# Performance work log

Measured on AMD Instinct MI355X. Metric: run time of the kernel, lower is better.

The kernel has to match this reference:

```python
import jax, jax.numpy as jnp
import numpy as np

N, E, B = 4096, 8192, 128


def seg_softmax(logits, seg, n):
    m = jax.ops.segment_max(logits, seg, num_segments=n)
    e = jnp.exp(logits - m[seg])
    s = jax.ops.segment_sum(e, seg, num_segments=n)
    return e / (s[seg] + 1e-16)


def gat(x, src, dst, W, a_src, a_dst, b, H, C, n):
    # PyG GATConv, concat=False (mean over heads), self-loops already appended
    h = (x @ W).reshape(n, H, C)
    al_s = jnp.sum(h * a_src, -1)  # [n,H]
    al_d = jnp.sum(h * a_dst, -1)
    logits = jax.nn.leaky_relu(al_s[src] + al_d[dst], 0.2)  # [E',H]
    alpha = seg_softmax(logits, dst, n)
    out = jax.ops.segment_sum(h[src] * alpha[:, :, None], dst, num_segments=n)
    return out.mean(1) + b


def gcn(x, src, dst, W, b, n):
    deg = jax.ops.segment_sum(jnp.ones_like(dst, jnp.float32), dst, num_segments=n)
    dis = jnp.where(deg > 0, deg ** -0.5, 0.0)
    norm = dis[src] * dis[dst]
    h = x @ W
    return jax.ops.segment_sum(h[src] * norm[:, None], dst, num_segments=n) + b


def transformer_conv(x, src, dst, Wq, bq, Wk, bk, Wv, bv, Ws, bs, H, C, n):
    # PyG TransformerConv, concat=False, root_weight=True, no self-loops
    q = (x @ Wq + bq).reshape(n, H, C)
    k = (x @ Wk + bk).reshape(n, H, C)
    v = (x @ Wv + bv).reshape(n, H, C)
    logits = jnp.sum(q[dst] * k[src], -1) / jnp.sqrt(jnp.float32(C))  # [E,H]
    alpha = seg_softmax(logits, dst, n)
    agg = jax.ops.segment_sum(v[src] * alpha[:, :, None], dst, num_segments=n)
    return agg.mean(1) + (x @ Ws + bs)


def gap(x, batch, nb):
    s = jax.ops.segment_sum(x, batch, num_segments=nb)
    cnt = jax.ops.segment_sum(jnp.ones(x.shape[0], x.dtype), batch, num_segments=nb)
    return s / jnp.maximum(cnt, 1.0)[:, None]


def setup_inputs() -> dict:
    key = jax.random.key(0)
    ks = iter(jax.random.split(key, 64))
    p = {}
    p['x'] = jax.random.normal(next(ks), (N, 78), jnp.float32)
    p['fp'] = (jax.random.uniform(next(ks), (B, 1489)) > 0.5).astype(jnp.float32)
    p['edge_index'] = jax.random.randint(next(ks), (2, E), 0, N, jnp.int32)
    p['batch'] = (jnp.arange(N, dtype=jnp.int32) // (N // B))
    def w(k, shp, fan):
        return jax.random.normal(k, shp, jnp.float32) * (1.0 / np.sqrt(fan))
    # GAT layers (in, out, heads=8)
    for name, ci, co in [('g1', 78, 2048), ('g2', 2048, 1024), ('g3', 1024, 512)]:
        p[name + '_w'] = w(next(ks), (ci, 8 * co), ci)
        p[name + '_as'] = w(next(ks), (8, co), co)
        p[name + '_ad'] = w(next(ks), (8, co), co)
        p[name + '_b'] = jnp.zeros((co,), jnp.float32)
    p['gcn_w'] = w(next(ks), (512, 256), 512)
    p['gcn_b'] = jnp.zeros((256,), jnp.float32)
    # TransformerConv 78->512, heads=4
    for nm in ['t_wq', 't_wk', 't_wv']:
        p[nm] = w(next(ks), (78, 4 * 512), 78)
    for nm in ['t_bq', 't_bk', 't_bv']:
        p[nm] = jnp.zeros((4 * 512,), jnp.float32)
    p['t_ws'] = w(next(ks), (78, 512), 78)
    p['t_bs'] = jnp.zeros((512,), jnp.float32)
    p['fc1_w'] = w(next(ks), (1489, 128), 1489); p['fc1_b'] = jnp.zeros((128,), jnp.float32)
    p['fc2_w'] = w(next(ks), (128, 256), 128); p['fc2_b'] = jnp.zeros((256,), jnp.float32)
    for nm, ci, co in [('b1', 1024, 256), ('b2', 256, 128), ('b3', 128, 64), ('b4', 64, 1)]:
        p[nm + '_w'] = w(next(ks), (ci, co), ci)
        p[nm + '_b'] = jnp.zeros((co,), jnp.float32)
    return p


def reference(x, fp, edge_index, batch,
              g1_w, g1_as, g1_ad, g1_b, g2_w, g2_as, g2_ad, g2_b,
              g3_w, g3_as, g3_ad, g3_b, gcn_w, gcn_b,
              t_wq, t_wk, t_wv, t_bq, t_bk, t_bv, t_ws, t_bs,
              fc1_w, fc1_b, fc2_w, fc2_b,
              b1_w, b1_b, b2_w, b2_b, b3_w, b3_b, b4_w, b4_b):
    n = x.shape[0]
    sl = jnp.arange(n, dtype=edge_index.dtype)
    src_sl = jnp.concatenate([edge_index[0], sl])  # with self loops (GAT/GCN)
    dst_sl = jnp.concatenate([edge_index[1], sl])
    h = jax.nn.relu(gat(x, src_sl, dst_sl, g1_w, g1_as, g1_ad, g1_b, 8, 2048, n))
    h = jax.nn.relu(gat(h, src_sl, dst_sl, g2_w, g2_as, g2_ad, g2_b, 8, 1024, n))
    h = jax.nn.relu(gat(h, src_sl, dst_sl, g3_w, g3_as, g3_ad, g3_b, 8, 512, n))
    h = gcn(h, src_sl, dst_sl, gcn_w, gcn_b, n)
    x_gat = gap(h, batch, B)  # [B,256]
    fpn = jax.nn.relu(fp @ fc1_w + fc1_b)
    fpn = jax.nn.relu(fpn @ fc2_w + fc2_b)  # [B,256]
    xt = jax.nn.relu(transformer_conv(x, edge_index[0], edge_index[1],
                                      t_wq, t_bq, t_wk, t_bk, t_wv, t_bv,
                                      t_ws, t_bs, 4, 512, n))
    x_trans = gap(xt, batch, B)  # [B,512]
    xc = jnp.concatenate([x_gat, x_trans, fpn], axis=1)  # [B,1024]
    h = jax.nn.relu(xc @ b1_w + b1_b)
    h = jax.nn.relu(h @ b2_w + b2_b)
    h = jax.nn.relu(h @ b3_w + b3_b)
    return jax.nn.sigmoid(h @ b4_w + b4_b)
```

## Files before the change

### kernel.cpp

```cpp
#include <hip/hip_runtime.h>

typedef unsigned short u16;
typedef unsigned int   u32;

typedef __bf16 bf16x8 __attribute__((ext_vector_type(8)));
typedef float  f32x4  __attribute__((ext_vector_type(4)));

#define NNODE 4096
#define NEDGE 8192
#define NEG   12288

__device__ __forceinline__ float blo(u32 u){ return __uint_as_float(u<<16); }
__device__ __forceinline__ float bhi(u32 u){ return __uint_as_float(u & 0xffff0000u); }
__device__ __forceinline__ u16 f2b(float f){
  u32 u = __float_as_uint(f);
  u += 0x7fffu + ((u>>16)&1u);
  return (u16)(u>>16);
}
__device__ __forceinline__ void split_bf(float a, u16& hi, u16& lo){
  u32 u = __float_as_uint(a);
  u32 r = u + 0x7fffu + ((u>>16)&1u);
  hi = (u16)(r>>16);
  float h = __uint_as_float(r & 0xffff0000u);
  float l = a - h;
  u32 u2 = __float_as_uint(l);
  lo = (u16)((u2 + 0x7fffu + ((u2>>16)&1u)) >> 16);
}
__device__ __forceinline__ u16 hi_bf(float a){
  u32 u = __float_as_uint(a);
  return (u16)((u + 0x7fffu + ((u>>16)&1u)) >> 16);
}

#define GL2LDS(g,l) __builtin_amdgcn_global_load_lds((const __attribute__((address_space(1))) unsigned int*)(g), (__attribute__((address_space(3))) unsigned int*)(l), 16, 0, 0)

__global__ __launch_bounds__(256) void zero_i(int* p, int n){
  int i = blockIdx.x*256 + threadIdx.x; if (i<n) p[i]=0;
}
__global__ __launch_bounds__(256) void hist_k(const int* __restrict__ ei, int* deg_g, int* deg_t){
  int e = blockIdx.x*256 + threadIdx.x; if (e>=NEG) return;
  int dv = (e<NEDGE) ? ei[NEDGE+e] : e-NEDGE;
  atomicAdd(&deg_g[dv],1);
  if (e<NEDGE) atomicAdd(&deg_t[dv],1);
}
__global__ __launch_bounds__(1024) void scan4096(const int* __restrict__ deg, int* __restrict__ off){
  __shared__ int lds[1024];
  int tid = threadIdx.x;
  int v[4]; int s=0;
  #pragma unroll
  for (int j=0;j<4;j++){ v[j]=deg[tid*4+j]; s+=v[j]; }
  lds[tid]=s; __syncthreads();
  for (int d=1; d<1024; d<<=1){
    int t = (tid>=d) ? lds[tid-d] : 0;
    __syncthreads();
    lds[tid] += t;
    __syncthreads();
  }
  int base = (tid>0) ? lds[tid-1] : 0;
  #pragma unroll
  for (int j=0;j<4;j++){ off[tid*4+j]=base; base+=v[j]; }
  if (tid==1023) off[4096]=base;
}
__global__ __launch_bounds__(256) void scatter_k(const int* __restrict__ ei,
    const int* __restrict__ off_g, int* cur_g, int* csr_g,
    const int* __restrict__ off_t, int* cur_t, int* csr_t){
  int e = blockIdx.x*256 + threadIdx.x; if (e>=NEG) return;
  int s, dv;
  if (e<NEDGE){ s=ei[e]; dv=ei[NEDGE+e]; } else { s=dv=e-NEDGE; }
  int p = atomicAdd(&cur_g[dv],1);
  csr_g[off_g[dv]+p]=s;
  if (e<NEDGE){ int p2 = atomicAdd(&cur_t[dv],1); csr_t[off_t[dv]+p2]=s; }
}
__global__ __launch_bounds__(256) void mkdis(const int* __restrict__ deg, float* dis){
  int i = blockIdx.x*256 + threadIdx.x; if (i>=NNODE) return;
  int d = deg[i]; dis[i] = d>0 ? rsqrtf((float)d) : 0.f;
}
__global__ __launch_bounds__(128) void pad_x(const float* __restrict__ x, float* __restrict__ xp,
                                             u16* __restrict__ xh){
  int n = blockIdx.x, c = threadIdx.x;
  if (c<96){
    float v = (c<78) ? x[(size_t)n*78+c] : 0.f;
    if (c<80) xp[(size_t)n*80+c] = v;
    xh[(size_t)n*96+c] = hi_bf(v);
  }
}
__global__ __launch_bounds__(256) void repack_w1(const float* __restrict__ g1w, float* __restrict__ w1r){
  int i = blockIdx.x*256 + threadIdx.x;
  int kk = i >> 11, c = i & 2047;
  int h = kk/80, k2 = kk - h*80;
  w1r[i] = (k2<78) ? g1w[(size_t)k2*16384 + h*2048 + c] : 0.f;
}

__global__ __launch_bounds__(256) void tpd(const float* __restrict__ in, int Ntot, int n0,
    int K, int Kp, u16* __restrict__ outh){
  __shared__ float t[32][33];
  int bx = blockIdx.x*32;
  int by = blockIdx.y*32;
  int tx = threadIdx.x & 31, ty = threadIdx.x >> 5;
  for (int i=ty;i<32;i+=8){
    int kk=by+i;
    t[i][tx] = (kk<K) ? in[(size_t)kk*Ntot + n0 + bx + tx] : 0.f;
  }
  __syncthreads();
  for (int i=ty;i<32;i+=8){
    int nn=bx+i, kk=by+tx;
    if (kk<Kp) outh[(size_t)nn*Kp+kk] = hi_bf(t[tx][i]);
  }
}

__global__ __launch_bounds__(256) void mk_wsT(const float* __restrict__ wsv, const float* __restrict__ wdv,
    u16* __restrict__ th, u16* __restrict__ tl, int Kp){
  int i = blockIdx.x*256 + threadIdx.x;
  if (i >= 16*Kp) return;
  int r = i / Kp, k = i - r*Kp;
  float v = (r<8) ? wsv[k*8+r] : wdv[k*8+(r-8)];
  u16 h,l; split_bf(v,h,l);
  th[i]=h; tl[i]=l;
}


template<int KS>
__global__ __launch_bounds__(256,4) void alk_mm(
    const u16* __restrict__ Ah, const u16* __restrict__ Al, int lda,
    const u16* __restrict__ Bh, const u16* __restrict__ Bl,
    float* __restrict__ alsd, int K)
{
  __shared__ __align__(16) u16 Ash[128*32], Asl[128*32], Bsh[16*32], Bsl[16*32];
  int tid = threadIdx.x, lane = tid & 63, wave = tid >> 6;
  int bm = blockIdx.y*128;
  int kb = blockIdx.x*(K/KS), ke = kb + K/KS;
  int m16 = lane & 15, quad = lane >> 4;
  int srow = lane >> 2;
  int skk = (((lane & 3) - (srow >> 1)) & 3) * 8;
  int kq  = (((quad + (m16 >> 1)) & 3)) * 8;
  f32x4 acc[2] = {};
  for (int k0=kb; k0<ke; k0+=32){
    __syncthreads();
    #pragma unroll
    for (int t=0;t<2;t++){
      int g = wave + t*4; int row = g*16 + srow;
      GL2LDS(Ah + (size_t)(bm+row)*lda + k0 + skk, &Ash[g*512]);
      GL2LDS(Al + (size_t)(bm+row)*lda + k0 + skk, &Asl[g*512]);
    }
    if (wave==0) GL2LDS(Bh + (size_t)srow*lda + k0 + skk, &Bsh[0]);
    if (wave==1) GL2LDS(Bl + (size_t)srow*lda + k0 + skk, &Bsl[0]);
    __syncthreads();
    bf16x8 bh = *(const bf16x8*)&Bsh[m16*32+kq];
    bf16x8 bl = *(const bf16x8*)&Bsl[m16*32+kq];
    #pragma unroll
    for (int i=0;i<2;i++){
      bf16x8 ah = *(const bf16x8*)&Ash[(wave*32+i*16+m16)*32+kq];
      bf16x8 al = *(const bf16x8*)&Asl[(wave*32+i*16+m16)*32+kq];
      acc[i] = __builtin_amdgcn_mfma_f32_16x16x32_bf16(ah, bh, acc[i],0,0,0);
      acc[i] = __builtin_amdgcn_mfma_f32_16x16x32_bf16(al, bh, acc[i],0,0,0);
      acc[i] = __builtin_amdgcn_mfma_f32_16x16x32_bf16(ah, bl, acc[i],0,0,0);
    }
  }
  #pragma unroll
  for (int i=0;i<2;i++){
    int row0 = bm + wave*32 + i*16 + quad*4;
    #pragma unroll
    for (int r=0;r<4;r++)
      atomicAdd(&alsd[(size_t)(row0+r)*16 + m16], acc[i][r]);
  }
}

#define BM 128
#define BN 128
template<int EPI, int SA, typename CT>
__global__ __launch_bounds__(256,4) void mgemm(
    const u16* __restrict__ Ah, const u16* __restrict__ Al, int lda,
    const u16* __restrict__ Bh, int ldb,
    CT* __restrict__ C, int ldc, int K,
    const float* __restrict__ bias, float scale,
    u16* __restrict__ Chi, u16* __restrict__ Clo)
{
  __shared__ __align__(16) u16 Ash[128*32];
  __shared__ __align__(16) u16 Bsh[128*32];
  __shared__ __align__(16) u16 Asl[SA?128*32:16];
  int tid = threadIdx.x;
  int bm = blockIdx.y*BM, bn = blockIdx.x*BN;
  int lane = tid & 63, wave = tid >> 6;
  int wr = (wave>>1)*64, wc = (wave&1)*64;
  int m16 = lane & 15, quad = lane >> 4;
  int srow = lane >> 2;
  int skk = (((lane & 3) - (srow >> 1)) & 3) * 8;
  int kq  = (((quad + (m16 >> 1)) & 3)) * 8;

  f32x4 acc[4][4] = {};
  for (int k0=0; k0<K; k0+=32){
    __syncthreads();
    #pragma unroll
    for (int t=0;t<2;t++){
      int g = wave + t*4;
      int row = g*16 + srow;
      GL2LDS(Ah + (size_t)(bm+row)*lda + k0 + skk, &Ash[g*512]);
      if (SA) GL2LDS(Al + (size_t)(bm+row)*lda + k0 + skk, &Asl[g*512]);
      GL2LDS(Bh + (size_t)(bn+row)*ldb + k0 + skk, &Bsh[g*512]);
    }
    __syncthreads();
    bf16x8 ah[4], al_[4], bh_[4];
    #pragma unroll
    for (int i=0;i<4;i++){
      ah[i]  = *(const bf16x8*)&Ash[(wr+i*16+m16)*32 + kq];
      if (SA) al_[i] = *(const bf16x8*)&Asl[(wr+i*16+m16)*32 + kq];
    }
    #pragma unroll
    for (int j=0;j<4;j++)
      bh_[j] = *(const bf16x8*)&Bsh[(wc+j*16+m16)*32 + kq];
    #pragma unroll
    for (int i=0;i<4;i++)
      #pragma unroll
      for (int j=0;j<4;j++){
        acc[i][j] = __builtin_amdgcn_mfma_f32_16x16x32_bf16(ah[i], bh_[j], acc[i][j], 0,0,0);
        if (SA) acc[i][j] = __builtin_amdgcn_mfma_f32_16x16x32_bf16(al_[i], bh_[j], acc[i][j], 0,0,0);
      }
  }
  #pragma unroll
  for (int i=0;i<4;i++){
    int row0 = bm + wr + i*16 + quad*4;
    #pragma unroll
    for (int j=0;j<4;j++){
      int col = bn + wc + j*16 + m16;
      float bv = (EPI==1||EPI==5) ? bias[col] : 0.f;
      #pragma unroll
      for (int r=0;r<4;r++){
        float v = acc[i][j][r];
        if constexpr (EPI==5){
          v = fmaxf(v*scale + bv, 0.f);
          size_t idx = (size_t)(row0+r)*ldc + col;
          u16 h_, l_; split_bf(v, h_, l_);
          Chi[idx]=h_; Clo[idx]=l_;
        } else {
          if (EPI==1) v += bv;
          size_t idx = (size_t)(row0+r)*ldc + col;
          if constexpr (sizeof(CT)==2) C[idx] = (CT)f2b(v);
          else C[idx] = (CT)v;
        }
      }
    }
  }
}

__device__ __forceinline__ void stA8(const u16* __restrict__ A, int lda, u16* dst,
                                     int bm, int kt, int h, int w, int lane){
  int q = ((lane&7) ^ (lane>>3)) * 8;
  #pragma unroll
  for (int t=0;t<2;t++){
    int rbase = t*128 + h*64 + w*8;
    int rl = rbase + (lane>>3);
    GL2LDS(A + (size_t)(bm+rl)*lda + kt*64 + q, dst + rbase*64);
  }
}
__device__ __forceinline__ void stB8(const u16* __restrict__ B, int ldb, u16* dst,
                                     int bn, int kt, int nh, int w, int lane){
  int q = ((lane&7) ^ (lane>>3)) * 8;
  #pragma unroll
  for (int t=0;t<2;t++){
    int rbase = (w>>1)*64 + nh*32 + (w&1)*16 + t*8;
    int rl = rbase + (lane>>3);
    GL2LDS(B + (size_t)(bn+rl)*ldb + kt*64 + q, dst + rbase*64);
  }
}
#define LDX8(BUF, ROW, KS) \
  (*(const bf16x8*)&(BUF)[(ROW)*64 + ((((KS)*4 + quad) ^ (m16 & 7)))*8])
#define RDA8(BUF, MH) \
  _Pragma("unroll") for (int mi=0;mi<4;mi++){ \
    a_[mi][0] = LDX8(BUF, wr*128 + ((MH)*4+mi)*16 + m16, 0); \
    a_[mi][1] = LDX8(BUF, wr*128 + ((MH)*4+mi)*16 + m16, 1); }
#define RDB8(BUF, NH, BB) \
  _Pragma("unroll") for (int nj=0;nj<2;nj++){ \
    BB[nj][0] = LDX8(BUF, wc*64 + ((NH)*2+nj)*16 + m16, 0); \
    BB[nj][1] = LDX8(BUF, wc*64 + ((NH)*2+nj)*16 + m16, 1); }
#define MMQ8(MH, NH, BB) \
  _Pragma("unroll") for (int mi=0;mi<4;mi++) \
    _Pragma("unroll") for (int nj=0;nj<2;nj++){ \
      acc[(MH)*4+mi][(NH)*2+nj] = __builtin_amdgcn_mfma_f32_16x16x32_bf16(a_[mi][0], BB[nj][0], acc[(MH)*4+mi][(NH)*2+nj],0,0,0); \
      acc[(MH)*4+mi][(NH)*2+nj] = __builtin_amdgcn_mfma_f32_16x16x32_bf16(a_[mi][1], BB[nj][1], acc[(MH)*4+mi][(NH)*2+nj],0,0,0); }
#define LGKM0 asm volatile("s_waitcnt lgkmcnt(0)" ::: "memory")
#define BAR   __builtin_amdgcn_s_barrier()

__global__ __launch_bounds__(512,2) void mgemm8(
    const u16* __restrict__ A, int lda,
    const u16* __restrict__ B, int ldb,
    u16* __restrict__ C, int ldc, int K, int nbx)
{
  __shared__ __align__(16) u16 As0[16384], As1[16384], Bs0[16384], Bs1[16384];
  int tid = threadIdx.x, lane = tid & 63, w = tid >> 6;
  int m16 = lane & 15, quad = lane >> 4;
  int wr = w >> 2, wc = w & 3;
  int nwg = (int)gridDim.x, bid = (int)blockIdx.x;
  int wg = (bid & 7)*(nwg>>3) + (bid>>3);
  int by = wg / nbx, bx = wg - by*nbx;
  int bm = by*256, bn = bx*256;
  int NT = K >> 6, NP = NT >> 1;
  f32x4 acc[8][4] = {};
  bf16x8 a_[4][2], b0_[2][2], b1_[2][2];
  stA8(A,lda,As0,bm,0,0,w,lane);
  stB8(B,ldb,Bs0,bn,0,0,w,lane);
  stB8(B,ldb,Bs0,bn,0,1,w,lane);
  stA8(A,lda,As0,bm,0,1,w,lane);
  stA8(A,lda,As1,bm,1,0,w,lane);
  stB8(B,ldb,Bs1,bn,1,0,w,lane);
  stB8(B,ldb,Bs1,bn,1,1,w,lane);
  stA8(A,lda,As1,bm,1,1,w,lane);
  asm volatile("s_waitcnt vmcnt(8)" ::: "memory");
  BAR;
  for (int i=0;i<NP;i++){
    int t2 = 2*i+2; if (t2>=NT) t2=NT-1;
    int t3 = 2*i+3; if (t3>=NT) t3=NT-1;
    RDA8(As0,0); RDB8(Bs0,0,b0_);
    asm volatile("s_waitcnt lgkmcnt(8)" ::: "memory");
    BAR; LGKM0;
    __builtin_amdgcn_s_setprio(1); MMQ8(0,0,b0_); __builtin_amdgcn_s_setprio(0);
    BAR;
    RDB8(Bs0,1,b1_);
    stA8(A,lda,As0,bm,t2,0,w,lane);
    stB8(B,ldb,Bs0,bn,t2,0,w,lane);
    BAR; LGKM0;
    __builtin_amdgcn_s_setprio(1); MMQ8(0,1,b1_); __builtin_amdgcn_s_setprio(0);
    BAR;
    RDA8(As0,1);
    stB8(B,ldb,Bs0,bn,t2,1,w,lane);
    BAR; LGKM0;
    __builtin_amdgcn_s_setprio(1); MMQ8(1,1,b1_); __builtin_amdgcn_s_setprio(0);
    BAR;
    stA8(A,lda,As0,bm,t2,1,w,lane);
    BAR;
    __builtin_amdgcn_s_setprio(1); MMQ8(1,0,b0_); __builtin_amdgcn_s_setprio(0);
    asm volatile("s_waitcnt vmcnt(8)" ::: "memory");
    BAR;
    RDA8(As1,0); RDB8(Bs1,0,b0_);
    asm volatile("s_waitcnt lgkmcnt(8)" ::: "memory");
    BAR; LGKM0;
    __builtin_amdgcn_s_setprio(1); MMQ8(0,0,b0_); __builtin_amdgcn_s_setprio(0);
    BAR;
    RDB8(Bs1,1,b1_);
    stA8(A,lda,As1,bm,t3,0,w,lane);
    stB8(B,ldb,Bs1,bn,t3,0,w,lane);
    BAR; LGKM0;
    __builtin_amdgcn_s_setprio(1); MMQ8(0,1,b1_); __builtin_amdgcn_s_setprio(0);
    BAR;
    RDA8(As1,1);
    stB8(B,ldb,Bs1,bn,t3,1,w,lane);
    BAR; LGKM0;
    __builtin_amdgcn_s_setprio(1); MMQ8(1,1,b1_); __builtin_amdgcn_s_setprio(0);
    BAR;
    stA8(A,lda,As1,bm,t3,1,w,lane);
    BAR;
    __builtin_amdgcn_s_setprio(1); MMQ8(1,0,b0_); __builtin_amdgcn_s_setprio(0);
    asm volatile("s_waitcnt vmcnt(8)" ::: "memory");
    BAR;
  }
  asm volatile("s_waitcnt vmcnt(0)" ::: "memory");
  #pragma unroll
  for (int mi=0;mi<8;mi++){
    int row0 = bm + wr*128 + mi*16 + quad*4;
    #pragma unroll
    for (int nj=0;nj<4;nj++){
      int col = bn + wc*64 + nj*16 + m16;
      #pragma unroll
      for (int r=0;r<4;r++)
        C[(size_t)(row0+r)*ldc + col] = f2b(acc[mi][nj][r]);
    }
  }
}

__global__ __launch_bounds__(256) void wsvec(const float* __restrict__ W,
    const float* __restrict__ as_, const float* __restrict__ ad_,
    float* __restrict__ ws, float* __restrict__ wd,
    int Kreal, int H, int C)
{
  int wv = blockIdx.x*4 + (threadIdx.x>>6);
  int lane = threadIdx.x & 63;
  int k = wv / H, h = wv - k*H;
  float ps=0.f, pd=0.f;
  if (k < Kreal){
    const float* wr = W + (size_t)k*((size_t)H*C) + (size_t)h*C;
    const float* ar = as_ + (size_t)h*C;
    const float* dr = ad_ + (size_t)h*C;
    for (int c=lane;c<C;c+=64){ float w=wr[c]; ps += w*ar[c]; pd += w*dr[c]; }
  }
  #pragma unroll
  for (int o=32;o;o>>=1){ ps += __shfl_down(ps,o); pd += __shfl_down(pd,o); }
  if (lane==0){ ws[k*H+h]=ps; wd[k*H+h]=pd; }
}
__global__ __launch_bounds__(256) void alk(const float* __restrict__ X,
    const float* __restrict__ ws, const float* __restrict__ wd,
    float* __restrict__ alsd, int Kp)
{
  int n = blockIdx.x, tid = threadIdx.x;
  int hh = tid>>5, l32 = tid&31;
  const float* xr = X + (size_t)n*Kp;
  float ps=0.f, pd=0.f;
  for (int k=l32;k<Kp;k+=32){
    float xv = xr[k];
    ps += xv*ws[k*8+hh];
    pd += xv*wd[k*8+hh];
  }
  #pragma unroll
  for (int o=16;o;o>>=1){ ps += __shfl_down(ps,o,32); pd += __shfl_down(pd,o,32); }
  if (l32==0){ alsd[n*16+hh]=ps; alsd[n*16+8+hh]=pd; }
}

__global__ __launch_bounds__(256) void gat1_gather(
    const float* __restrict__ xpad, const float* __restrict__ alsd,
    const int* __restrict__ off, const int* __restrict__ csr,
    u16* __restrict__ y1h, u16* __restrict__ y1l)
{
  int d = blockIdx.x, tid = threadIdx.x;
  int hh = tid>>5, l32 = tid&31;
  int e0 = off[d], e1 = off[d+1];
  __shared__ float mh[8], lih[8], adh[8];
  __shared__ float wl[32][8];
  __shared__ int sl[32];
  if (tid < 8){
    float ad = alsd[d*16+8+tid]; adh[tid]=ad;
    float m=-1e30f, l=0.f;
    for (int e=e0;e<e1;++e){
      float xv = alsd[csr[e]*16+tid] + ad;
      xv = xv>0.f?xv:0.2f*xv;
      if (xv>m){ l = l*__expf(m-xv)+1.f; m=xv; } else l += __expf(xv-m);
    }
    mh[tid]=m; lih[tid]=1.f/l;
  }
  __syncthreads();
  float acc0=0.f, acc1=0.f, acc2v=0.f;
  for (int cb=e0; cb<e1; cb+=32){
    int ce = min(32, e1-cb);
    if (tid < ce*8){
      int j = tid>>3, h2 = tid&7;
      int s = csr[cb+j];
      if (h2==0) sl[j]=s;
      float xv = alsd[s*16+h2] + adh[h2];
      xv = xv>0.f?xv:0.2f*xv;
      wl[j][h2] = __expf(xv-mh[h2])*lih[h2];
    }
    __syncthreads();
    for (int j=0;j<ce;++j){
      float w = wl[j][hh];
      const float* xr = xpad + (size_t)sl[j]*80;
      acc0 += w*xr[l32];
      acc1 += w*xr[l32+32];
      if (l32 < 16) acc2v += w*xr[l32+64];
    }
    __syncthreads();
  }
  size_t base = (size_t)d*640 + hh*80;
  u16 h_, l_;
  split_bf(acc0, h_, l_); y1h[base+l32]=h_;    y1l[base+l32]=l_;
  split_bf(acc1, h_, l_); y1h[base+l32+32]=h_; y1l[base+l32+32]=l_;
  if (l32<16){ split_bf(acc2v, h_, l_); y1h[base+l32+64]=h_; y1l[base+l32+64]=l_; }
}

template<int HPC, int C>
__global__ __launch_bounds__(256) void gat_aggN(
    const u16* __restrict__ h, const float* __restrict__ alsd,
    const int* __restrict__ off, const int* __restrict__ csr,
    float* __restrict__ accum, int head0)
{
  constexpr int V = C/256;
  int d = blockIdx.x, tid = threadIdx.x;
  int e0=off[d], e1=off[d+1];
  __shared__ float mh[HPC], lih[HPC], adh[HPC];
  __shared__ float wl[32][HPC];
  __shared__ int sl[32];
  if (tid < HPC){
    float ad = alsd[d*16 + 8 + head0 + tid]; adh[tid]=ad;
    float m=-1e30f,l=0.f;
    for (int e=e0;e<e1;++e){
      float xv = alsd[csr[e]*16 + head0 + tid]+ad;
      xv = xv>0.f?xv:0.2f*xv;
      if (xv>m){ l=l*__expf(m-xv)+1.f; m=xv; } else l+=__expf(xv-m);
    }
    mh[tid]=m; lih[tid]=1.f/l;
  }
  __syncthreads();
  float acc[HPC][V];
  #pragma unroll
  for (int a=0;a<HPC;a++)
    #pragma unroll
    for (int v=0;v<V;v++) acc[a][v]=0.f;
  int c0 = tid*V;
  for (int cb=e0;cb<e1;cb+=32){
    int ce = min(32, e1-cb);
    if (tid < ce*HPC){
      int j = tid/HPC, h2 = tid - j*HPC;
      int s = csr[cb+j];
      if (h2==0) sl[j]=s;
      float xv = alsd[s*16 + head0 + h2] + adh[h2];
      xv = xv>0.f?xv:0.2f*xv;
      wl[j][h2] = __expf(xv-mh[h2])*lih[h2];
    }
    __syncthreads();
    for (int j=0;j<ce;++j){
      const u16* hr = h + (size_t)sl[j]*(HPC*C);
      #pragma unroll
      for (int a=0;a<HPC;a++){
        float w = wl[j][a];
        if constexpr (V==4){
          uint2 u = *(const uint2*)(hr + a*C + c0);
          acc[a][0] += w*blo(u.x); acc[a][1] += w*bhi(u.x);
          acc[a][2] += w*blo(u.y); acc[a][3] += w*bhi(u.y);
        } else {
          u32 u = *(const u32*)(hr + a*C + c0);
          acc[a][0] += w*blo(u); acc[a][1] += w*bhi(u);
        }
      }
    }
    __syncthreads();
  }
  float* ar = accum + (size_t)d*C + c0;
  #pragma unroll
  for (int v=0;v<V;v++){
    float s2 = 0.f;
    #pragma unroll
    for (int a=0;a<HPC;a++) s2 += acc[a][v];
    ar[v] += s2;
  }
}
__global__ __launch_bounds__(256) void finishx(const float* __restrict__ accum,
    const float* __restrict__ bias, float* __restrict__ xo, int Cmask){
  int i = blockIdx.x*256 + threadIdx.x;
  int c = i & Cmask;
  xo[i] = fmaxf(accum[i]*0.125f + bias[c], 0.f);
}
__global__ __launch_bounds__(256) void finishx2(const float* __restrict__ accum,
    const float* __restrict__ bias,
    u16* __restrict__ xh, u16* __restrict__ xl, int Cmask){
  int i = blockIdx.x*256 + threadIdx.x;
  int c = i & Cmask;
  float v = fmaxf(accum[i]*0.125f + bias[c], 0.f);
  u16 h_, l_; split_bf(v, h_, l_);
  xh[i]=h_; xl[i]=l_;
}

__global__ __launch_bounds__(256) void pool_gcn(const float* __restrict__ x3,
    const float* __restrict__ dis, const int* __restrict__ off, const int* __restrict__ csr,
    float* __restrict__ z)
{
  int g = blockIdx.x, tid = threadIdx.x;
  int c0 = tid*2;
  float a0=0.f, a1=0.f;
  for (int dd=0; dd<32; ++dd){
    int d = g*32+dd;
    int e0=off[d], e1=off[d+1];
    float b0=0.f, b1=0.f;
    for (int e=e0;e<e1;++e){
      int s = csr[e]; float ds = dis[s];
      const float* xr = x3 + (size_t)s*512 + c0;
      b0 += ds*xr[0]; b1 += ds*xr[1];
    }
    float dw = dis[d];
    a0 += dw*b0; a1 += dw*b1;
  }
  z[(size_t)g*512+c0]   = a0*(1.f/32.f);
  z[(size_t)g*512+c0+1] = a1*(1.f/32.f);
}

__global__ __launch_bounds__(256) void tr_agg(
  const u16* __restrict__ qkvs, const int* __restrict__ off, const int* __restrict__ csr,
  float* __restrict__ xt)
{
  int d = blockIdx.x, tid = threadIdx.x;
  int wv = tid>>6, lane = tid&63;
  int e0=off[d], e1=off[d+1];
  __shared__ float osum[4][512];
  __shared__ float sp[4][64];
  float qf[8];
  { uint4 u = *(const uint4*)(qkvs + (size_t)d*6656 + wv*512 + lane*8);
    qf[0]=blo(u.x); qf[1]=bhi(u.x); qf[2]=blo(u.y); qf[3]=bhi(u.y);
    qf[4]=blo(u.z); qf[5]=bhi(u.z); qf[6]=blo(u.w); qf[7]=bhi(u.w); }
  const float scale = 0.04419417382415922f;
  float m=-1e30f,l=0.f;
  for (int e=e0;e<e1;++e){
    int s = csr[e];
    uint4 u = *(const uint4*)(qkvs + (size_t)s*6656 + 2048 + wv*512 + lane*8);
    float p = qf[0]*blo(u.x)+qf[1]*bhi(u.x)+qf[2]*blo(u.y)+qf[3]*bhi(u.y)
            + qf[4]*blo(u.z)+qf[5]*bhi(u.z)+qf[6]*blo(u.w)+qf[7]*bhi(u.w);
    #pragma unroll
    for (int o=32;o;o>>=1) p += __shfl_xor(p,o);
    p *= scale;
    int idx = e-e0;
    if (lane==0 && idx<64) sp[wv][idx]=p;
    if (p>m){ l=l*__expf(m-p)+1.f; m=p; } else l+=__expf(p-m);
  }
  float li = (e1>e0)?1.f/l:0.f;
  float acc[8]={0.f,0.f,0.f,0.f,0.f,0.f,0.f,0.f};
  for (int e=e0;e<e1;++e){
    int s = csr[e];
    int idx = e-e0;
    float p;
    if (idx<64) p = sp[wv][idx];
    else {
      uint4 u = *(const uint4*)(qkvs + (size_t)s*6656 + 2048 + wv*512 + lane*8);
      p = qf[0]*blo(u.x)+qf[1]*bhi(u.x)+qf[2]*blo(u.y)+qf[3]*bhi(u.y)
        + qf[4]*blo(u.z)+qf[5]*bhi(u.z)+qf[6]*blo(u.w)+qf[7]*bhi(u.w);
      #pragma unroll
      for (int o=32;o;o>>=1) p += __shfl_xor(p,o);
      p *= scale;
    }
    float w = __expf(p - m)*li;
    uint4 u = *(const uint4*)(qkvs + (size_t)s*6656 + 4096 + wv*512 + lane*8);
    acc[0]+=w*blo(u.x); acc[1]+=w*bhi(u.x); acc[2]+=w*blo(u.y); acc[3]+=w*bhi(u.y);
    acc[4]+=w*blo(u.z); acc[5]+=w*bhi(u.z); acc[6]+=w*blo(u.w); acc[7]+=w*bhi(u.w);
  }
  #pragma unroll
  for (int j=0;j<8;j++) osum[wv][lane*8+j]=acc[j];
  __syncthreads();
  for (int c=tid;c<512;c+=256){
    u16 sk = qkvs[(size_t)d*6656 + 6144 + c];
    float o = (osum[0][c]+osum[1][c]+osum[2][c]+osum[3][c])*0.25f + blo((u32)sk);
    xt[(size_t)d*512+c] = fmaxf(o,0.f);
  }
}

__global__ __launch_bounds__(256) void catb(const float* __restrict__ bq, const float* __restrict__ bk,
    const float* __restrict__ bv, const float* __restrict__ bs, float* __restrict__ o){
  int i = blockIdx.x*256 + threadIdx.x; if (i>=6656) return;
  float v;
  if (i<2048) v=bq[i]; else if (i<4096) v=bk[i-2048];
  else if (i<6144) v=bv[i-4096]; else v=bs[i-6144];
  o[i]=v;
}

__device__ __forceinline__ float dotb(const u16* __restrict__ w, const float* __restrict__ s,
                                      int k0, int k1){
  float acc=0.f;
  #pragma unroll 4
  for (int k=k0;k<k1;k+=8){
    uint4 u = *(const uint4*)(w+k);
    float4 s0 = *(const float4*)(s+k);
    float4 s1 = *(const float4*)(s+k+4);
    acc += blo(u.x)*s0.x + bhi(u.x)*s0.y + blo(u.y)*s0.z + bhi(u.y)*s0.w
         + blo(u.z)*s1.x + bhi(u.z)*s1.y + blo(u.w)*s1.z + bhi(u.w)*s1.w;
  }
  return acc;
}
__global__ __launch_bounds__(256) void head_k(
  const float* __restrict__ z, const float* __restrict__ xt, const float* __restrict__ fp,
  const u16* __restrict__ gcnT, const float* __restrict__ gcn_b,
  const u16* __restrict__ fc1T, const float* __restrict__ fc1_b,
  const u16* __restrict__ fc2T, const float* __restrict__ fc2_b,
  const u16* __restrict__ b1T, const float* __restrict__ b1_b,
  const u16* __restrict__ b2T, const float* __restrict__ b2_b,
  const u16* __restrict__ b3T, const float* __restrict__ b3_b,
  const float* __restrict__ b4_w, const float* __restrict__ b4_b,
  float* __restrict__ out)
{
  int g = blockIdx.x, tid = threadIdx.x;
  __shared__ __align__(16) float xc[1024];
  __shared__ __align__(16) float sa[1504];
  __shared__ __align__(16) float sb[256];
  __shared__ __align__(16) float scm[256];
  for (int c=tid;c<512;c+=256) sa[c] = z[(size_t)g*512+c];
  __syncthreads();
  float vgcn = gcn_b[tid] + dotb(gcnT + (size_t)tid*512, sa, 0, 512);
  for (int c=tid;c<512;c+=256){
    float s=0.f;
    for (int i=0;i<32;i++) s += xt[(size_t)(g*32+i)*512 + c];
    xc[256+c] = s*(1.f/32.f);
  }
  xc[tid] = vgcn;
  __syncthreads();
  for (int c=tid;c<1496;c+=256) sa[c] = (c<1489) ? fp[(size_t)g*1489+c] : 0.f;
  __syncthreads();
  { int n = tid & 127, half = tid >> 7;
    sb[tid] = dotb(fc1T + (size_t)n*1496, sa, half?752:0, half?1496:752); }
  __syncthreads();
  if (tid<128) scm[tid] = fmaxf(sb[tid]+sb[tid+128]+fc1_b[tid], 0.f);
  __syncthreads();
  xc[768+tid] = fmaxf(fc2_b[tid] + dotb(fc2T + (size_t)tid*128, scm, 0, 128), 0.f);
  __syncthreads();
  sa[tid] = fmaxf(b1_b[tid] + dotb(b1T + (size_t)tid*1024, xc, 0, 1024), 0.f);
  __syncthreads();
  { int n = tid & 127, half = tid >> 7;
    sb[tid] = dotb(b2T + (size_t)n*256, sa, half*128, half*128+128); }
  __syncthreads();
  if (tid<128) scm[tid] = fmaxf(sb[tid]+sb[tid+128]+b2_b[tid], 0.f);
  __syncthreads();
  { int n = tid & 63, part = tid >> 6;
    sb[tid] = dotb(b3T + (size_t)n*128, scm, part*32, part*32+32); }
  __syncthreads();
  if (tid<64) sa[tid] = fmaxf(sb[tid]+sb[tid+64]+sb[tid+128]+sb[tid+192]+b3_b[tid], 0.f);
  __syncthreads();
  if (tid<64){
    float p = sa[tid]*b4_w[tid];
    #pragma unroll
    for (int o=32;o;o>>=1) p += __shfl_down(p,o);
    if (tid==0) out[g] = 1.f/(1.f+__expf(-(p + b4_b[0])));
  }
}

extern "C" void kernel_launch(void* const* d_in, const int* in_sizes, int n_in,
                              void* d_out, int out_size, void* d_ws, size_t ws_size,
                              hipStream_t stream)
{
  (void)in_sizes; (void)n_in; (void)out_size; (void)ws_size;
  const float* x     = (const float*)d_in[0];
  const float* fp    = (const float*)d_in[1];
  const int*   ei    = (const int*)d_in[2];
  const float* g1_w  = (const float*)d_in[4];
  const float* g1_as = (const float*)d_in[5];
  const float* g1_ad = (const float*)d_in[6];
  const float* g1_b  = (const float*)d_in[7];
  const float* g2_w  = (const float*)d_in[8];
  const float* g2_as = (const float*)d_in[9];
  const float* g2_ad = (const float*)d_in[10];
  const float* g2_b  = (const float*)d_in[11];
  const float* g3_w  = (const float*)d_in[12];
  const float* g3_as = (const float*)d_in[13];
  const float* g3_ad = (const float*)d_in[14];
  const float* g3_b  = (const float*)d_in[15];
  const float* gcn_w = (const float*)d_in[16];
  const float* gcn_b = (const float*)d_in[17];
  const float* t_wq  = (const float*)d_in[18];
  const float* t_wk  = (const float*)d_in[19];
  const float* t_wv  = (const float*)d_in[20];
  const float* t_bq  = (const float*)d_in[21];
  const float* t_bk  = (const float*)d_in[22];
  const float* t_bv  = (const float*)d_in[23];
  const float* t_ws  = (const float*)d_in[24];
  const float* t_bs  = (const float*)d_in[25];
  const float* fc1_w = (const float*)d_in[26];
  const float* fc1_b = (const float*)d_in[27];
  const float* fc2_w = (const float*)d_in[28];
  const float* fc2_b = (const float*)d_in[29];
  const float* b1_w  = (const float*)d_in[30];
  const float* b1_b  = (const float*)d_in[31];
  const float* b2_w  = (const float*)d_in[32];
  const float* b2_b  = (const float*)d_in[33];
  const float* b3_w  = (const float*)d_in[34];
  const float* b3_b  = (const float*)d_in[35];
  const float* b4_w  = (const float*)d_in[36];
  const float* b4_b  = (const float*)d_in[37];

  char* base = (char*)d_ws;
  size_t offb = 0;
  auto alloc = [&](size_t bytes)->void*{
    void* p = base + offb; offb = (offb + bytes + 255) & ~(size_t)255; return p;
  };
  int*   cnt   = (int*)alloc(16384*4);
  int*   off_g = (int*)alloc(4097*4);
  int*   off_t = (int*)alloc(4097*4);
  int*   csr_g = (int*)alloc(12288*4);
  int*   csr_t = (int*)alloc(8192*4);
  float* dis   = (float*)alloc(4096*4);
  float* xpad  = (float*)alloc((size_t)4096*80*4);
  u16*   xph   = (u16*)alloc((size_t)4096*96*2);
  float* alsd  = (float*)alloc((size_t)4096*16*4);
  float* wsv   = (float*)alloc((size_t)2048*8*4);
  float* wdv   = (float*)alloc((size_t)2048*8*4);
  u16*   wsTh  = (u16*)alloc((size_t)16*2048*2);
  u16*   wsTl  = (u16*)alloc((size_t)16*2048*2);
  float* zbuf  = (float*)alloc((size_t)128*512*4);
  float* cbias = (float*)alloc((size_t)6656*4);
  float* w1r   = (float*)alloc((size_t)640*2048*4);
  u16*   gcnT  = (u16*)alloc((size_t)256*512*2);
  u16*   fc1T  = (u16*)alloc((size_t)128*1496*2);
  u16*   fc2T  = (u16*)alloc((size_t)256*128*2);
  u16*   b1T   = (u16*)alloc((size_t)256*1024*2);
  u16*   b2T   = (u16*)alloc((size_t)128*256*2);
  u16*   b3T   = (u16*)alloc((size_t)64*128*2);
  char*  big   = (char*)alloc((size_t)140<<20);

  u16*   y1h   = (u16*)  (big);
  u16*   y1l   = (u16*)  (big + ((size_t)5<<20));
  u16*   w1rth = (u16*)  (big + ((size_t)10<<20));
  u16*   x1h   = (u16*)  (big + ((size_t)16<<20));
  u16*   x1l   = (u16*)  (big + ((size_t)32<<20));
  u16*   w2th  = (u16*)  (big + ((size_t)48<<20));
  u16*   h2    = (u16*)  (big + ((size_t)64<<20));
  float* acc2  = (float*)(big + ((size_t)96<<20));
  u16*   x2h   = (u16*)  (big + ((size_t)112<<20));
  u16*   x2l   = (u16*)  (big + ((size_t)120<<20));
  u16*   w3th  = (u16*)  (big);
  u16*   h3    = (u16*)  (big + ((size_t)8<<20));
  float* acc3  = (float*)(big + ((size_t)40<<20));
  float* x3    = (float*)(big + ((size_t)48<<20));
  u16*   qkvTh = (u16*)  (big);
  u16*   qkvs  = (u16*)  (big + ((size_t)8<<20));
  float* xt    = (float*)(big + ((size_t)64<<20));

  int* deg_g = cnt;       int* cur_g = cnt+4096;
  int* deg_t = cnt+8192;  int* cur_t = cnt+12288;

  zero_i<<<64,256,0,stream>>>(cnt, 16384);
  hist_k<<<48,256,0,stream>>>(ei, deg_g, deg_t);
  scan4096<<<1,1024,0,stream>>>(deg_g, off_g);
  scan4096<<<1,1024,0,stream>>>(deg_t, off_t);
  scatter_k<<<48,256,0,stream>>>(ei, off_g, cur_g, csr_g, off_t, cur_t, csr_t);
  mkdis<<<16,256,0,stream>>>(deg_g, dis);
  pad_x<<<4096,128,0,stream>>>(x, xpad, xph);
  repack_w1<<<5120,256,0,stream>>>(g1_w, w1r);
  tpd<<<dim3(8,16),256,0,stream>>>(gcn_w, 256, 0, 512, 512, gcnT);
  tpd<<<dim3(4,47),256,0,stream>>>(fc1_w, 128, 0, 1489, 1496, fc1T);
  tpd<<<dim3(8,4), 256,0,stream>>>(fc2_w, 256, 0, 128, 128, fc2T);
  tpd<<<dim3(8,32),256,0,stream>>>(b1_w,  256, 0, 1024, 1024, b1T);
  tpd<<<dim3(4,8), 256,0,stream>>>(b2_w,  128, 0, 256, 256, b2T);
  tpd<<<dim3(2,4), 256,0,stream>>>(b3_w,  64,  0, 128, 128, b3T);

  wsvec<<<160,256,0,stream>>>(g1_w, g1_as, g1_ad, wsv, wdv, 78, 8, 2048);
  alk<<<4096,256,0,stream>>>(xpad, wsv, wdv, alsd, 80);
  gat1_gather<<<4096,256,0,stream>>>(xpad, alsd, off_g, csr_g, y1h, y1l);
  tpd<<<dim3(64,20),256,0,stream>>>(w1r, 2048, 0, 640, 640, w1rth);
  mgemm<5,1,float><<<dim3(16,32),256,0,stream>>>(y1h, y1l, 640, w1rth, 640,
                                         nullptr, 2048, 640, g1_b, 0.125f, x1h, x1l);

  wsvec<<<4096,256,0,stream>>>(g2_w, g2_as, g2_ad, wsv, wdv, 2048, 8, 1024);
  mk_wsT<<<128,256,0,stream>>>(wsv, wdv, wsTh, wsTl, 2048);
  hipMemsetAsync(alsd, 0, (size_t)4096*16*4, stream);
  alk_mm<8><<<dim3(8,32),256,0,stream>>>(x1h, x1l, 2048, wsTh, wsTl, alsd, 2048);
  hipMemsetAsync(acc2, 0, (size_t)4096*1024*4, stream);
  for (int c=0;c<2;c++){
    tpd<<<dim3(128,64),256,0,stream>>>(g2_w, 8192, c*4096, 2048, 2048, w2th);
    mgemm8<<<256,512,0,stream>>>(x1h, 2048, w2th, 2048, h2, 4096, 2048, 16);
    gat_aggN<4,1024><<<4096,256,0,stream>>>(h2, alsd, off_g, csr_g, acc2, c*4);
  }
  finishx2<<<16384,256,0,stream>>>(acc2, g2_b, x2h, x2l, 1023);

  wsvec<<<2048,256,0,stream>>>(g3_w, g3_as, g3_ad, wsv, wdv, 1024, 8, 512);
  mk_wsT<<<64,256,0,stream>>>(wsv, wdv, wsTh, wsTl, 1024);
  hipMemsetAsync(alsd, 0, (size_t)4096*16*4, stream);
  alk_mm<8><<<dim3(8,32),256,0,stream>>>(x2h, x2l, 1024, wsTh, wsTl, alsd, 1024);
  hipMemsetAsync(acc3, 0, (size_t)4096*512*4, stream);
  tpd<<<dim3(128,32),256,0,stream>>>(g3_w, 4096, 0, 1024, 1024, w3th);
  mgemm8<<<256,512,0,stream>>>(x2h, 1024, w3th, 1024, h3, 4096, 1024, 16);
  gat_aggN<8,512><<<4096,256,0,stream>>>(h3, alsd, off_g, csr_g, acc3, 0);
  finishx<<<8192,256,0,stream>>>(acc3, g3_b, x3, 511);
  pool_gcn<<<128,256,0,stream>>>(x3, dis, off_g, csr_g, zbuf);

  tpd<<<dim3(64,3),256,0,stream>>>(t_wq, 2048, 0, 78, 96, qkvTh);
  tpd<<<dim3(64,3),256,0,stream>>>(t_wk, 2048, 0, 78, 96, qkvTh + (size_t)2048*96);
  tpd<<<dim3(64,3),256,0,stream>>>(t_wv, 2048, 0, 78, 96, qkvTh + (size_t)4096*96);
  tpd<<<dim3(16,3),256,0,stream>>>(t_ws, 512,  0, 78, 96, qkvTh + (size_t)6144*96);
  catb<<<26,256,0,stream>>>(t_bq, t_bk, t_bv, t_bs, cbias);
  mgemm<1,0,u16><<<dim3(52,32),256,0,stream>>>(xph, nullptr, 96, qkvTh, 96,
                                         qkvs, 6656, 96, cbias, 0.f, nullptr, nullptr);
  tr_agg<<<4096,256,0,stream>>>(qkvs, off_t, csr_t, xt);

  head_k<<<128,256,0,stream>>>(zbuf, xt, fp, gcnT, gcn_b,
                               fc1T, fc1_b, fc2T, fc2_b,
                               b1T, b1_b, b2T, b2_b, b3T, b3_b, b4_w, b4_b,
                               (float*)d_out);
}
```

Baseline: 767.4 us.

## Double-buffer A fragments and overlap LDS reads with MFMA phases in mgemm8

Restructures the main loop of the bf16 MFMA GEMM into uniform phases. Each phase issues LDS fragment reads for the next phase and a global-to-LDS stage before running the current MFMA block, using two A register sets and rotating B sets. It drops the explicit lgkmcnt waits and the extra barrier, and adds sched_barrier to stop the compiler reordering across phases. This aims to hide LDS latency behind matrix work. In exchange it uses more registers, and the LDS hazard ordering depends on the compiler inserting waits correctly.

```diff
diff --git a/kernel.cpp b/kernel.cpp
--- a/kernel.cpp
+++ b/kernel.cpp
@@ -263,21 +263,26 @@
 }
 #define LDX8(BUF, ROW, KS) \
   (*(const bf16x8*)&(BUF)[(ROW)*64 + ((((KS)*4 + quad) ^ (m16 & 7)))*8])
-#define RDA8(BUF, MH) \
+#define RDA8(BUF, MH, AA) \
   _Pragma("unroll") for (int mi=0;mi<4;mi++){ \
-    a_[mi][0] = LDX8(BUF, wr*128 + ((MH)*4+mi)*16 + m16, 0); \
-    a_[mi][1] = LDX8(BUF, wr*128 + ((MH)*4+mi)*16 + m16, 1); }
+    AA[mi][0] = LDX8(BUF, wr*128 + ((MH)*4+mi)*16 + m16, 0); \
+    AA[mi][1] = LDX8(BUF, wr*128 + ((MH)*4+mi)*16 + m16, 1); }
 #define RDB8(BUF, NH, BB) \
   _Pragma("unroll") for (int nj=0;nj<2;nj++){ \
     BB[nj][0] = LDX8(BUF, wc*64 + ((NH)*2+nj)*16 + m16, 0); \
     BB[nj][1] = LDX8(BUF, wc*64 + ((NH)*2+nj)*16 + m16, 1); }
-#define MMQ8(MH, NH, BB) \
+#define MMQ8(MH, NH, AA, BB) \
   _Pragma("unroll") for (int mi=0;mi<4;mi++) \
     _Pragma("unroll") for (int nj=0;nj<2;nj++){ \
-      acc[(MH)*4+mi][(NH)*2+nj] = __builtin_amdgcn_mfma_f32_16x16x32_bf16(a_[mi][0], BB[nj][0], acc[(MH)*4+mi][(NH)*2+nj],0,0,0); \
-      acc[(MH)*4+mi][(NH)*2+nj] = __builtin_amdgcn_mfma_f32_16x16x32_bf16(a_[mi][1], BB[nj][1], acc[(MH)*4+mi][(NH)*2+nj],0,0,0); }
-#define LGKM0 asm volatile("s_waitcnt lgkmcnt(0)" ::: "memory")
+      acc[(MH)*4+mi][(NH)*2+nj] = __builtin_amdgcn_mfma_f32_16x16x32_bf16(AA[mi][0], BB[nj][0], acc[(MH)*4+mi][(NH)*2+nj],0,0,0); \
+      acc[(MH)*4+mi][(NH)*2+nj] = __builtin_amdgcn_mfma_f32_16x16x32_bf16(AA[mi][1], BB[nj][1], acc[(MH)*4+mi][(NH)*2+nj],0,0,0); }
 #define BAR   __builtin_amdgcn_s_barrier()
+#define SBAR  __builtin_amdgcn_sched_barrier(0)
+#define VM8   asm volatile("s_waitcnt vmcnt(8)" ::: "memory")
+#define MMPH(MH,NH,AA,BB) \
+  SBAR; BAR; \
+  __builtin_amdgcn_s_setprio(1); MMQ8(MH,NH,AA,BB); __builtin_amdgcn_s_setprio(0); \
+  VM8; BAR;
 
 __global__ __launch_bounds__(512,2) void mgemm8(
     const u16* __restrict__ A, int lda,
@@ -294,7 +299,7 @@
   int bm = by*256, bn = bx*256;
   int NT = K >> 6, NP = NT >> 1;
   f32x4 acc[8][4] = {};
-  bf16x8 a_[4][2], b0_[2][2], b1_[2][2];
+  bf16x8 aA[4][2], aB[4][2], b0_[2][2], b1_[2][2];
   stA8(A,lda,As0,bm,0,0,w,lane);
   stB8(B,ldb,Bs0,bn,0,0,w,lane);
   stB8(B,ldb,Bs0,bn,0,1,w,lane);
@@ -302,54 +307,37 @@
   stA8(A,lda,As1,bm,1,0,w,lane);
   stB8(B,ldb,Bs1,bn,1,0,w,lane);
   stB8(B,ldb,Bs1,bn,1,1,w,lane);
-  stA8(A,lda,As1,bm,1,1,w,lane);
-  asm volatile("s_waitcnt vmcnt(8)" ::: "memory");
+  VM8;
   BAR;
+  RDA8(As0,0,aA); RDB8(Bs0,0,b0_);
   for (int i=0;i<NP;i++){
-    int t2 = 2*i+2; if (t2>=NT) t2=NT-1;
-    int t3 = 2*i+3; if (t3>=NT) t3=NT-1;
-    RDA8(As0,0); RDB8(Bs0,0,b0_);
-    asm volatile("s_waitcnt lgkmcnt(8)" ::: "memory");
-    BAR; LGKM0;
-    __builtin_amdgcn_s_setprio(1); MMQ8(0,0,b0_); __builtin_amdgcn_s_setprio(0);
-    BAR;
+    int t2 = 2*i+2; if (t2>NT-1) t2=NT-1;
+    int t3 = 2*i+3; if (t3>NT-1) t3=NT-1;
+    int t3p = 2*i+1;
     RDB8(Bs0,1,b1_);
+    stA8(A,lda,As1,bm,t3p,1,w,lane);
+    MMPH(0,0,aA,b0_);
+    RDA8(As0,1,aB);
     stA8(A,lda,As0,bm,t2,0,w,lane);
+    MMPH(0,1,aA,b1_);
+    RDA8(As1,0,aA);
     stB8(B,ldb,Bs0,bn,t2,0,w,lane);
-    BAR; LGKM0;
-    __builtin_amdgcn_s_setprio(1); MMQ8(0,1,b1_); __builtin_amdgcn_s_setprio(0);
-    BAR;
-    RDA8(As0,1);
+    MMPH(1,1,aB,b1_);
+    RDB8(Bs1,0,b1_);
     stB8(B,ldb,Bs0,bn,t2,1,w,lane);
-    BAR; LGKM0;
-    __builtin_amdgcn_s_setprio(1); MMQ8(1,1,b1_); __builtin_amdgcn_s_setprio(0);
-    BAR;
+    MMPH(1,0,aB,b0_);
+    RDB8(Bs1,1,b0_);
     stA8(A,lda,As0,bm,t2,1,w,lane);
-    BAR;
-    __builtin_amdgcn_s_setprio(1); MMQ8(1,0,b0_); __builtin_amdgcn_s_setprio(0);
-    asm volatile("s_waitcnt vmcnt(8)" ::: "memory");
-    BAR;
-    RDA8(As1,0); RDB8(Bs1,0,b0_);
-    asm volatile("s_waitcnt lgkmcnt(8)" ::: "memory");
-    BAR; LGKM0;
-    __builtin_amdgcn_s_setprio(1); MMQ8(0,0,b0_); __builtin_amdgcn_s_setprio(0);
-    BAR;
-    RDB8(Bs1,1,b1_);
+    MMPH(0,0,aA,b1_);
+    RDA8(As1,1,aB);
     stA8(A,lda,As1,bm,t3,0,w,lane);
+    MMPH(0,1,aA,b0_);
+    RDA8(As0,0,aA);
     stB8(B,ldb,Bs1,bn,t3,0,w,lane);
-    BAR; LGKM0;
-    __builtin_amdgcn_s_setprio(1); MMQ8(0,1,b1_); __builtin_amdgcn_s_setprio(0);
-    BAR;
-    RDA8(As1,1);
+    MMPH(1,1,aB,b0_);
+    RDB8(Bs0,0,b0_);
     stB8(B,ldb,Bs1,bn,t3,1,w,lane);
-    BAR; LGKM0;
-    __builtin_amdgcn_s_setprio(1); MMQ8(1,1,b1_); __builtin_amdgcn_s_setprio(0);
-    BAR;
-    stA8(A,lda,As1,bm,t3,1,w,lane);
-    BAR;
-    __builtin_amdgcn_s_setprio(1); MMQ8(1,0,b0_); __builtin_amdgcn_s_setprio(0);
-    asm volatile("s_waitcnt vmcnt(8)" ::: "memory");
-    BAR;
+    MMPH(1,0,aB,b1_);
   }
   asm volatile("s_waitcnt vmcnt(0)" ::: "memory");
   #pragma unroll
```

Result: slower. 1.017 ms (+32.5%).
